# Kernel tuning notes

Hardware: AMD Instinct MI355X
Metric: run time of the kernel (lower is better)

## Reference

```python
import jax, jax.numpy as jnp
import numpy as np

WINDOW_SIZE = 11
PAD = WINDOW_SIZE // 2


def _box_filter(x):
    """Depthwise uniform box filter, separable: two 1D convs with 1/W weights.

    x: [N, C, H, W] float. Zero padding of PAD on each side (matches torch
    F.conv2d(padding=PAD) with the outer-product uniform window).
    """
    c = x.shape[1]
    w = jnp.full((c, 1, WINDOW_SIZE, 1), 1.0 / WINDOW_SIZE, dtype=x.dtype)
    # vertical pass
    y = jax.lax.conv_general_dilated(
        x, w, window_strides=(1, 1), padding=((PAD, PAD), (0, 0)),
        dimension_numbers=('NCHW', 'OIHW', 'NCHW'), feature_group_count=c)
    # horizontal pass
    w2 = jnp.transpose(w, (0, 1, 3, 2))  # [C,1,1,WINDOW_SIZE]
    y = jax.lax.conv_general_dilated(
        y, w2, window_strides=(1, 1), padding=((0, 0), (PAD, PAD)),
        dimension_numbers=('NCHW', 'OIHW', 'NCHW'), feature_group_count=c)
    return y


def _ssim_loss(img1, img2):
    C1 = 0.01 ** 2
    C2 = 0.03 ** 2
    mu1 = _box_filter(img1)
    mu2 = _box_filter(img2)
    mu1_sq = mu1 * mu1
    mu2_sq = mu2 * mu2
    mu1_mu2 = mu1 * mu2
    sigma1_sq = _box_filter(img1 * img1) - mu1_sq
    sigma2_sq = _box_filter(img2 * img2) - mu2_sq
    sigma12 = _box_filter(img1 * img2) - mu1_mu2
    ssim_map = ((2 * mu1_mu2 + C1) * (2 * sigma12 + C2)) / (
        (mu1_sq + mu2_sq + C1) * (sigma1_sq + sigma2_sq + C2))
    return 1.0 - jnp.mean(ssim_map)


def setup_inputs() -> dict:
    key = jax.random.key(0)
    k1, k2 = jax.random.split(key)
    shape = (16, 3, 512, 512)
    img1 = jax.random.uniform(k1, shape, dtype=jnp.float32)
    img2 = jax.random.uniform(k2, shape, dtype=jnp.float32)
    return {"img1": img1, "img2": img2}


def reference(img1, img2):
    return _ssim_loss(img1, img2)
```

## Files before the change

kernel.cpp:

```cpp
#include <hip/hip_runtime.h>
#include <math.h>


typedef __fp16 half2_t __attribute__((ext_vector_type(2)));

constexpr int WIN  = 11;
constexpr int OTW  = 116;
constexpr int OTH  = 32;
constexpr int VP   = 127;
constexpr int SEGR = 8;
constexpr int SEGI = SEGR + WIN - 1;
constexpr int GPW  = 15;
constexpr int H = 512, W = 512;
constexpr int NPLANES = 16 * 3;
constexpr int GRIDX = (W + OTW - 1) / OTW;
constexpr long long NPIX = (long long)NPLANES * H * W;

__device__ __forceinline__ float ssim_px(float ws, float wd, float wss, float wdd) {
    const float C1 = 1e-4f;
    const float C2 = 9e-4f;
    const float k1 = 1.0f / 121.0f;
    const float c2a = 0.5f * k1 * k1;
    const float c2c = 0.5f * k1;
    const float P = (c2a * ws) * ws;
    const float Q = (c2a * wd) * wd;
    const float U = c2c * wss;
    const float T = c2c * wdd;
    const float r1 = P - Q;
    const float p1 = P + Q;
    const float t1 = U - T;
    const float u1 = U + T;
    const float num = (r1 + C1) * (t1 - r1 + C2);
    const float den = (p1 + C1) * (u1 - p1 + C2);
    return num * __builtin_amdgcn_rcpf(den);
}

__device__ __forceinline__ float ssim2(half2_t asd, half2_t asq) {
    return ssim_px((float)asd[0], (float)asd[1], (float)asq[0], (float)asq[1]);
}

template<bool XE, bool YE>
__device__ __forceinline__ void vpass(const float* __restrict__ ca,
                                      const float* __restrict__ cb,
                                      int gy0, bool xok0, bool xok1,
                                      int vrow0, int lane,
                                      half2_t (*V)[VP][2]) {
    half2_t r0[WIN], r1[WIN];
    half2_t asd0 = {(__fp16)0, (__fp16)0}, asq0 = asd0;
    half2_t asd1 = asd0, asq1 = asd0;
#pragma unroll
    for (int r = 0; r < SEGI; ++r) {
        float a0, a1, b0, b1;
        if (YE) {
            const int gy = gy0 + r;
            a0 = a1 = b0 = b1 = 0.f;
            if ((unsigned)gy < (unsigned)H) {
                const float2 va = *(const float2*)(ca + (size_t)gy * W);
                const float2 vb = *(const float2*)(cb + (size_t)gy * W);
                a0 = va.x; a1 = va.y; b0 = vb.x; b1 = vb.y;
            }
        } else {
            const float2 va = *(const float2*)(ca + (size_t)(gy0 + r) * W);
            const float2 vb = *(const float2*)(cb + (size_t)(gy0 + r) * W);
            a0 = va.x; a1 = va.y; b0 = vb.x; b1 = vb.y;
        }
        if (XE) {
            a0 = xok0 ? a0 : 0.f;  b0 = xok0 ? b0 : 0.f;
            a1 = xok1 ? a1 : 0.f;  b1 = xok1 ? b1 : 0.f;
        }
        const int i = r % WIN;
        const half2_t p0 = __builtin_amdgcn_cvt_pkrtz(a0 + b0, a0 - b0);
        const half2_t p1 = __builtin_amdgcn_cvt_pkrtz(a1 + b1, a1 - b1);
        asd0 += p0;  asq0 += p0 * p0;
        asd1 += p1;  asq1 += p1 * p1;
        if (r >= WIN) {
            const half2_t o0 = r0[i], o1 = r1[i];
            asd0 -= o0;  asq0 -= o0 * o0;
            asd1 -= o1;  asq1 -= o1 * o1;
        }
        r0[i] = p0;  r1[i] = p1;
        if (r >= WIN - 1) {
            const int vr = vrow0 + r - (WIN - 1);
            V[vr][2 * lane][0]     = asd0;
            V[vr][2 * lane][1]     = asq0;
            V[vr][2 * lane + 1][0] = asd1;
            V[vr][2 * lane + 1][1] = asq1;
        }
    }
}

template<bool CHK>
__device__ __forceinline__ float hpass(const half2_t (*V)[VP][2], int row,
                                       int x0, int gxb) {
    half2_t asd = {(__fp16)0, (__fp16)0}, asq = asd;
#pragma unroll
    for (int r = 0; r < WIN; ++r) {
        asd += V[row][x0 + 1 + r][0];
        asq += V[row][x0 + 1 + r][1];
    }
    float local = 0.0f;
    if (!CHK || gxb < W)
        local = ssim2(asd, asq);
#pragma unroll
    for (int k = 1; k < GPW; ++k) {
        asd += V[row][x0 + k + WIN][0] - V[row][x0 + k][0];
        asq += V[row][x0 + k + WIN][1] - V[row][x0 + k][1];
        if ((x0 + k < OTW) && (!CHK || gxb + k < W))
            local += ssim2(asd, asq);
    }
    return local;
}

__global__ __launch_bounds__(256, 5)
void ssim_tile_kernel(const float* __restrict__ img1,
                      const float* __restrict__ img2,
                      float* __restrict__ partials) {
    __shared__ half2_t V[OTH][VP][2];
    __shared__ float wsum[4];

    const int tid  = threadIdx.x;
    const int wave = tid >> 6;
    const int lane = tid & 63;
    const int tx0 = blockIdx.x * OTW;
    const int ty0 = blockIdx.y * OTH;
    const int plane = blockIdx.z;
    const float* __restrict__ pa = img1 + (size_t)plane * H * W;
    const float* __restrict__ pb = img2 + (size_t)plane * H * W;

    {
        const int gxl = tx0 - 6 + 2 * lane;
        const bool xok0 = (unsigned)gxl < (unsigned)W;
        const bool xok1 = (unsigned)(gxl + 1) < (unsigned)W;
        const int gc = min(max(gxl, 0), W - 2);
        const int gy0 = ty0 + wave * SEGR - (WIN / 2);
        const int vrow0 = wave * SEGR;
        const bool xe = (blockIdx.x == 0) || (blockIdx.x == GRIDX - 1);
        const bool ye = (gy0 < 0) || (gy0 + SEGI > H);
        const float* __restrict__ ca = pa + gc;
        const float* __restrict__ cb = pb + gc;
        if (!xe) {
            if (!ye) vpass<false, false>(ca, cb, gy0, xok0, xok1, vrow0, lane, V);
            else     vpass<false, true >(ca, cb, gy0, xok0, xok1, vrow0, lane, V);
        } else {
            if (!ye) vpass<true, false>(ca, cb, gy0, xok0, xok1, vrow0, lane, V);
            else     vpass<true, true >(ca, cb, gy0, xok0, xok1, vrow0, lane, V);
        }
    }
    __syncthreads();

    const int row = tid & 31;
    const int x0  = (tid >> 5) * GPW;
    const int gxb = tx0 + x0;
    float local;
    if (blockIdx.x != GRIDX - 1)
        local = hpass<false>(V, row, x0, gxb);
    else
        local = hpass<true >(V, row, x0, gxb);

    for (int off = 32; off > 0; off >>= 1)
        local += __shfl_down(local, off);
    if (lane == 0) wsum[wave] = local;
    __syncthreads();
    if (tid == 0) {
        const int bid = (blockIdx.z * gridDim.y + blockIdx.y) * gridDim.x + blockIdx.x;
        partials[bid] = wsum[0] + wsum[1] + wsum[2] + wsum[3];
    }
}

__global__ __launch_bounds__(1024)
void ssim_reduce_kernel(const float4* __restrict__ partials4, int n4,
                        float* __restrict__ out) {
    double s = 0.0;
    for (int i = threadIdx.x; i < n4; i += 1024) {
        const float4 p = partials4[i];
        s += (double)p.x + (double)p.y + (double)p.z + (double)p.w;
    }
    for (int off = 32; off > 0; off >>= 1)
        s += __shfl_down(s, off);
    __shared__ double wsum[16];
    if ((threadIdx.x & 63) == 0) wsum[threadIdx.x >> 6] = s;
    __syncthreads();
    if (threadIdx.x == 0) {
        double total = 0.0;
        for (int w = 0; w < 16; ++w) total += wsum[w];
        out[0] = (float)(1.0 - total / (double)NPIX);
    }
}

extern "C" void kernel_launch(void* const* d_in, const int* in_sizes, int n_in,
                              void* d_out, int out_size, void* d_ws, size_t ws_size,
                              hipStream_t stream) {
    const float* img1 = (const float*)d_in[0];
    const float* img2 = (const float*)d_in[1];
    float* out = (float*)d_out;
    float* partials = (float*)d_ws;

    dim3 grid(GRIDX, H / OTH, NPLANES);
    dim3 block(256);
    ssim_tile_kernel<<<grid, block, 0, stream>>>(img1, img2, partials);

    const int nblocks = GRIDX * (H / OTH) * NPLANES;
    ssim_reduce_kernel<<<1, 1024, 0, stream>>>((const float4*)partials,
                                               nblocks / 4, out);
}
```

Before: 36.67 us.

## Stage input rows in LDS once per block before the vertical pass

Each block now loads its 42 input rows once, converting them to packed half sum/diff, and stores them in a shared-memory staging buffer. The vertical pass then reads from LDS instead of global memory. Before, each wave reloaded 18 rows, so the 10 halo rows between adjacent waves were fetched redundantly. The cost is an extra LDS buffer and barrier, and the occupancy hint drops from 5 to 3 blocks per SIMD.

Measured after the change: 62.36 us. +70.1%, slower.

```diff
diff --git a/kernel.cpp b/kernel.cpp
--- a/kernel.cpp
+++ b/kernel.cpp
@@ -7,6 +7,7 @@
 constexpr int WIN  = 11;
 constexpr int OTW  = 116;
 constexpr int OTH  = 32;
+constexpr int INH  = OTH + WIN - 1;
 constexpr int VP   = 127;
 constexpr int SEGR = 8;
 constexpr int SEGI = SEGR + WIN - 1;
@@ -39,48 +40,56 @@
     return ssim_px((float)asd[0], (float)asd[1], (float)asq[0], (float)asq[1]);
 }
 
-template<bool XE, bool YE>
-__device__ __forceinline__ void vpass(const float* __restrict__ ca,
-                                      const float* __restrict__ cb,
-                                      int gy0, bool xok0, bool xok1,
-                                      int vrow0, int lane,
+template<bool XE>
+__device__ __forceinline__ void stage(const float* __restrict__ pa,
+                                      const float* __restrict__ pb,
+                                      int ty0, int gc, bool xok0, bool xok1,
+                                      int quad, int lane,
+                                      half2_t (*SD)[64][2]) {
+    const half2_t z = {(__fp16)0, (__fp16)0};
+#pragma unroll
+    for (int k = 0; k < (INH + 3) / 4; ++k) {
+        const int r = quad + 4 * k;
+        if (r < INH) {
+            const int gy = ty0 + r - (WIN / 2);
+            half2_t p0 = z, p1 = z;
+            if ((unsigned)gy < (unsigned)H) {
+                const float2 va = *(const float2*)(pa + (size_t)gy * W + gc);
+                const float2 vb = *(const float2*)(pb + (size_t)gy * W + gc);
+                p0 = __builtin_amdgcn_cvt_pkrtz(va.x + vb.x, va.x - vb.x);
+                p1 = __builtin_amdgcn_cvt_pkrtz(va.y + vb.y, va.y - vb.y);
+                if (XE) {
+                    p0 = xok0 ? p0 : z;
+                    p1 = xok1 ? p1 : z;
+                }
+            }
+            SD[r][lane][0] = p0;
+            SD[r][lane][1] = p1;
+        }
+    }
+}
+
+__device__ __forceinline__ void vpass(const half2_t (*SD)[64][2],
+                                      int wave, int lane,
                                       half2_t (*V)[VP][2]) {
     half2_t r0[WIN], r1[WIN];
     half2_t asd0 = {(__fp16)0, (__fp16)0}, asq0 = asd0;
     half2_t asd1 = asd0, asq1 = asd0;
+    const int base = wave * SEGR;
 #pragma unroll
     for (int r = 0; r < SEGI; ++r) {
-        float a0, a1, b0, b1;
-        if (YE) {
-            const int gy = gy0 + r;
-            a0 = a1 = b0 = b1 = 0.f;
-            if ((unsigned)gy < (unsigned)H) {
-                const float2 va = *(const float2*)(ca + (size_t)gy * W);
-                const float2 vb = *(const float2*)(cb + (size_t)gy * W);
-                a0 = va.x; a1 = va.y; b0 = vb.x; b1 = vb.y;
-            }
-        } else {
-            const float2 va = *(const float2*)(ca + (size_t)(gy0 + r) * W);
-            const float2 vb = *(const float2*)(cb + (size_t)(gy0 + r) * W);
-            a0 = va.x; a1 = va.y; b0 = vb.x; b1 = vb.y;
-        }
-        if (XE) {
-            a0 = xok0 ? a0 : 0.f;  b0 = xok0 ? b0 : 0.f;
-            a1 = xok1 ? a1 : 0.f;  b1 = xok1 ? b1 : 0.f;
-        }
-        const int i = r % WIN;
-        const half2_t p0 = __builtin_amdgcn_cvt_pkrtz(a0 + b0, a0 - b0);
-        const half2_t p1 = __builtin_amdgcn_cvt_pkrtz(a1 + b1, a1 - b1);
+        const half2_t p0 = SD[base + r][lane][0];
+        const half2_t p1 = SD[base + r][lane][1];
         asd0 += p0;  asq0 += p0 * p0;
         asd1 += p1;  asq1 += p1 * p1;
         if (r >= WIN) {
-            const half2_t o0 = r0[i], o1 = r1[i];
+            const half2_t o0 = r0[r % WIN], o1 = r1[r % WIN];
             asd0 -= o0;  asq0 -= o0 * o0;
             asd1 -= o1;  asq1 -= o1 * o1;
         }
-        r0[i] = p0;  r1[i] = p1;
+        r0[r % WIN] = p0;  r1[r % WIN] = p1;
         if (r >= WIN - 1) {
-            const int vr = vrow0 + r - (WIN - 1);
+            const int vr = base + r - (WIN - 1);
             V[vr][2 * lane][0]     = asd0;
             V[vr][2 * lane][1]     = asq0;
             V[vr][2 * lane + 1][0] = asd1;
@@ -111,10 +120,11 @@
     return local;
 }
 
-__global__ __launch_bounds__(256, 5)
+__global__ __launch_bounds__(256, 3)
 void ssim_tile_kernel(const float* __restrict__ img1,
                       const float* __restrict__ img2,
                       float* __restrict__ partials) {
+    __shared__ half2_t SD[INH][64][2];
     __shared__ half2_t V[OTH][VP][2];
     __shared__ float wsum[4];
 
@@ -132,20 +142,14 @@
         const bool xok0 = (unsigned)gxl < (unsigned)W;
         const bool xok1 = (unsigned)(gxl + 1) < (unsigned)W;
         const int gc = min(max(gxl, 0), W - 2);
-        const int gy0 = ty0 + wave * SEGR - (WIN / 2);
-        const int vrow0 = wave * SEGR;
-        const bool xe = (blockIdx.x == 0) || (blockIdx.x == GRIDX - 1);
-        const bool ye = (gy0 < 0) || (gy0 + SEGI > H);
-        const float* __restrict__ ca = pa + gc;
-        const float* __restrict__ cb = pb + gc;
-        if (!xe) {
-            if (!ye) vpass<false, false>(ca, cb, gy0, xok0, xok1, vrow0, lane, V);
-            else     vpass<false, true >(ca, cb, gy0, xok0, xok1, vrow0, lane, V);
-        } else {
-            if (!ye) vpass<true, false>(ca, cb, gy0, xok0, xok1, vrow0, lane, V);
-            else     vpass<true, true >(ca, cb, gy0, xok0, xok1, vrow0, lane, V);
-        }
-    }
+        if ((blockIdx.x == 0) || (blockIdx.x == GRIDX - 1))
+            stage<true >(pa, pb, ty0, gc, xok0, xok1, wave, lane, SD);
+        else
+            stage<false>(pa, pb, ty0, gc, xok0, xok1, wave, lane, SD);
+    }
+    __syncthreads();
+
+    vpass(SD, wave, lane, V);
     __syncthreads();
 
     const int row = tid & 31;
```
